# Optimization experiments

Hardware: AMD Instinct MI355X
Metric: run time of the kernel (lower is better)

Reference implementation:

```python
import jax, jax.numpy as jnp
import numpy as np

B, S, D, H, MLP = 2, 2048, 1024, 16, 4096
DH = D // H
EPS_LN = 1e-6
KERNEL_EPS = 1e-3  # fast_attention generalized kernel_epsilon


def layer_norm(x, scale, bias):
    m = jnp.mean(x, axis=-1, keepdims=True)
    v = jnp.mean(jnp.square(x - m), axis=-1, keepdims=True)
    return (x - m) * jax.lax.rsqrt(v + EPS_LN) * scale + bias


def performer_causal_attention(q, k, v):
    """FAVOR+ generalized attention (deterministic relu features), causal.

    q,k,v: [B,S,H,DH]. phi(x) = relu(x) + eps. Linear-time via prefix sums:
      out_i = phi(q_i) . cumsum_j<=i phi(k_j) v_j^T / (phi(q_i) . cumsum phi(k_j))
    """
    phi_q = jax.nn.relu(q) + KERNEL_EPS          # [B,S,H,M]
    phi_k = jax.nn.relu(k) + KERNEL_EPS          # [B,S,H,M]
    kv = jnp.cumsum(jnp.einsum('bshm,bshd->bshmd', phi_k, v), axis=1)  # [B,S,H,M,DH]
    num = jnp.einsum('bshm,bshmd->bshd', phi_q, kv)
    den = jnp.einsum('bshm,bshm->bsh', phi_q, jnp.cumsum(phi_k, axis=1))
    return num / den[..., None]


def setup_inputs() -> dict:
    key = jax.random.key(0)
    ks = jax.random.split(key, 7)
    def w(k, shape, scale):
        return jax.random.normal(k, shape, jnp.float32) * scale
    s_in = 1.0 / np.sqrt(D)
    return {
        'inputs': jax.random.normal(ks[0], (B, S, D), jnp.float32),
        'ln1_scale': jnp.ones((D,), jnp.float32),
        'ln1_bias': jnp.zeros((D,), jnp.float32),
        'wq': w(ks[1], (D, H, DH), s_in),
        'wk': w(ks[2], (D, H, DH), s_in),
        'wv': w(ks[3], (D, H, DH), s_in),
        'wo': w(ks[4], (H, DH, D), s_in),
        'ln2_scale': jnp.ones((D,), jnp.float32),
        'ln2_bias': jnp.zeros((D,), jnp.float32),
        'w1': w(ks[5], (D, MLP), s_in),
        'b1': jnp.zeros((MLP,), jnp.float32),
        'w2': w(ks[6], (MLP, D), 1.0 / np.sqrt(MLP)),
        'b2': jnp.zeros((D,), jnp.float32),
    }


def reference(inputs, ln1_scale, ln1_bias, wq, wk, wv, wo,
              ln2_scale, ln2_bias, w1, b1, w2, b2):
    # pre-LN self-attention (Performer FAVOR+ generalized, causal)
    x = layer_norm(inputs, ln1_scale, ln1_bias)
    q = jnp.einsum('bsd,dhm->bshm', x, wq)
    k = jnp.einsum('bsd,dhm->bshm', x, wk)
    v = jnp.einsum('bsd,dhm->bshm', x, wv)
    attn = performer_causal_attention(q, k, v)          # [B,S,H,DH]
    attn_out = jnp.einsum('bshm,hmd->bsd', attn, wo)    # output projection
    x = attn_out + inputs                               # residual
    # pre-LN MLP block
    y = layer_norm(x, ln2_scale, ln2_bias)
    y = jax.nn.gelu(y @ w1 + b1) @ w2 + b2
    return x + y
```

## Files before the change

kernel.cpp:

```cpp
#include <hip/hip_runtime.h>
#include <math.h>
#include <stdint.h>

typedef __bf16 bf16;
typedef bf16  bf16x8 __attribute__((ext_vector_type(8)));
typedef float f32x4  __attribute__((ext_vector_type(4)));

constexpr int Bb  = 2;
constexpr int Ss  = 2048;
constexpr int Dd  = 1024;
constexpr int Hh  = 16;
constexpr int DHh = 64;
constexpr int MLPd = 4096;
constexpr int ROWS = Bb * Ss;
constexpr int NC  = Ss / 64;
constexpr int BH  = Bb * Hh;
constexpr float EPS_LN = 1e-6f;
constexpr float KEPS   = 1e-3f;

__device__ __forceinline__ void async_copy16(const bf16* g, bf16* l) {
    __builtin_amdgcn_global_load_lds(
        (__attribute__((address_space(1))) void*)g,
        (__attribute__((address_space(3))) void*)l,
        16, 0, 0);
}

__device__ __forceinline__ int swz64(int row, int col) {
    return row * 64 + (((col >> 3) ^ row) & 7) * 8 + (col & 7);
}

__global__ __launch_bounds__(256) void preproc_kernel(
    const float* __restrict__ inputs,
    const float* __restrict__ ln1_scale, const float* __restrict__ ln1_bias,
    bf16* __restrict__ xln, bf16* __restrict__ inp_bf,
    const float* __restrict__ wq, const float* __restrict__ wk,
    const float* __restrict__ wv, const float* __restrict__ wo,
    bf16* __restrict__ wqT, bf16* __restrict__ wkT,
    bf16* __restrict__ wvT, bf16* __restrict__ woT,
    const float* __restrict__ w1, bf16* __restrict__ w1T,
    const float* __restrict__ w2, bf16* __restrict__ w2T)
{
    __shared__ float tile[32][33];
    __shared__ float ssum[4], ssq[4];
    const int blk = blockIdx.x;
    const int sector = blk >> 12;

    if (sector == 0) {
        const int row = blk;
        const float* xr = inputs + (size_t)row * Dd;
        const int c0 = threadIdx.x * 4;
        float vals[4];
        float sum = 0.f, sumsq = 0.f;
#pragma unroll
        for (int i = 0; i < 4; i++) {
            float v = xr[c0 + i];
            vals[i] = v;
            sum += v;
            sumsq += v * v;
        }
#pragma unroll
        for (int off = 32; off > 0; off >>= 1) {
            sum   += __shfl_down(sum, off);
            sumsq += __shfl_down(sumsq, off);
        }
        const int wave = threadIdx.x >> 6;
        if ((threadIdx.x & 63) == 0) { ssum[wave] = sum; ssq[wave] = sumsq; }
        __syncthreads();
        const float tot   = ssum[0] + ssum[1] + ssum[2] + ssum[3];
        const float totsq = ssq[0] + ssq[1] + ssq[2] + ssq[3];
        const float mean = tot * (1.f / Dd);
        const float var  = totsq * (1.f / Dd) - mean * mean;
        const float r = rsqrtf(var + EPS_LN);
        bf16* orow = xln + (size_t)row * Dd;
        bf16* irow = inp_bf + (size_t)row * Dd;
#pragma unroll
        for (int i = 0; i < 4; i++) {
            irow[c0 + i] = (bf16)vals[i];
            orow[c0 + i] = (bf16)((vals[i] - mean) * r * ln1_scale[c0 + i] + ln1_bias[c0 + i]);
        }
    } else {
        const float* in; bf16* out; int K, N, bx, by;
        if (sector == 1) {
            const int local = blk - 4096;
            const int z = local >> 10;
            in  = (z == 0) ? wq : (z == 1) ? wk : (z == 2) ? wv : wo;
            out = (z == 0) ? wqT : (z == 1) ? wkT : (z == 2) ? wvT : woT;
            K = 1024; N = 1024;
            bx = local & 31; by = (local >> 5) & 31;
        } else if (sector == 2) {
            const int local = blk - 8192;
            in = w1; out = w1T; K = 1024; N = 4096;
            bx = local & 127; by = local >> 7;
        } else {
            const int local = blk - 12288;
            in = w2; out = w2T; K = 4096; N = 1024;
            bx = local & 31; by = local >> 5;
        }
        const int k0 = by * 32, n0 = bx * 32;
        const int tx = threadIdx.x & 31, ty = threadIdx.x >> 5;
#pragma unroll
        for (int i = 0; i < 32; i += 8)
            tile[ty + i][tx] = in[(size_t)(k0 + ty + i) * N + n0 + tx];
        __syncthreads();
#pragma unroll
        for (int i = 0; i < 32; i += 8)
            out[(size_t)(n0 + ty + i) * K + k0 + tx] = (bf16)tile[tx][ty + i];
    }
}

__global__ __launch_bounds__(256) void wo_reduce_ln(
    const float* __restrict__ psA, const float* __restrict__ psB,
    const bf16* __restrict__ inp,
    const float* __restrict__ scale, const float* __restrict__ bias,
    bf16* __restrict__ x2, bf16* __restrict__ yln)
{
    const int row = blockIdx.x;
    const int c0 = threadIdx.x * 4;
    const size_t base = (size_t)row * Dd + c0;
    float vals[4];
    float sum = 0.f, sumsq = 0.f;
#pragma unroll
    for (int i = 0; i < 4; i++) {
        float v = psA[base + i] + psB[base + i] + (float)inp[base + i];
        v = (float)(bf16)v;
        vals[i] = v;
        sum += v;
        sumsq += v * v;
    }
#pragma unroll
    for (int off = 32; off > 0; off >>= 1) {
        sum   += __shfl_down(sum, off);
        sumsq += __shfl_down(sumsq, off);
    }
    __shared__ float ssum[4], ssq[4];
    const int wave = threadIdx.x >> 6;
    if ((threadIdx.x & 63) == 0) { ssum[wave] = sum; ssq[wave] = sumsq; }
    __syncthreads();
    const float tot   = ssum[0] + ssum[1] + ssum[2] + ssum[3];
    const float totsq = ssq[0] + ssq[1] + ssq[2] + ssq[3];
    const float mean = tot * (1.f / Dd);
    const float var  = totsq * (1.f / Dd) - mean * mean;
    const float r = rsqrtf(var + EPS_LN);
#pragma unroll
    for (int i = 0; i < 4; i++) {
        x2[base + i]  = (bf16)vals[i];
        yln[base + i] = (bf16)((vals[i] - mean) * r * scale[c0 + i] + bias[c0 + i]);
    }
}

__global__ __launch_bounds__(256) void mlp2_reduce(
    float* __restrict__ outp, const float* __restrict__ psB,
    const float* __restrict__ b2, const bf16* __restrict__ x2)
{
    const size_t i4 = ((size_t)blockIdx.x * 256 + threadIdx.x) * 4;
    const int col = (int)(i4 & 1023);
    f32x4 a = *(const f32x4*)&outp[i4];
    f32x4 b = *(const f32x4*)&psB[i4];
    f32x4 o;
#pragma unroll
    for (int j = 0; j < 4; j++)
        o[j] = a[j] + b[j] + b2[col + j] + (float)x2[i4 + j];
    *(f32x4*)&outp[i4] = o;
}

enum { EP_QKV = 0, EP_NONE = 1, EP_RES = 2, EP_GELU = 3, EP_BIAS_RES = 4, EP_PARTIAL = 5 };

template <int TN, int BK, int NDIM, int KDIM, int MODE, int KSPLIT>
__global__ __launch_bounds__(256, 2) void mfma_gemm(const bf16* __restrict__ A,
                                                    const bf16* __restrict__ BT,
                                                    void* __restrict__ Cout,
                                                    const float* __restrict__ bias,
                                                    const void* __restrict__ res,
                                                    bf16* __restrict__ out2,
                                                    bf16* __restrict__ out3)
{
    constexpr int WCT = TN / 2;
    constexpr int NJ  = TN / 32;
    constexpr int NS  = BK / 32;
    constexpr int CPR = BK / 8;
    constexpr int RPI = 2048 / BK;
    constexpr int GRIDY = 32;
    constexpr int RPX = GRIDY / 8;
    constexpr int TILES = GRIDY * (NDIM / TN);
    constexpr int KLEN  = KDIM / KSPLIT;
    __shared__ bf16 As[128 * BK];
    __shared__ bf16 Bs[TN * BK];
    const int t = threadIdx.x;
    const int wave = t >> 6, lane = t & 63;

    const int bid0 = blockIdx.x;
    const int ks  = (KSPLIT > 1) ? (bid0 / TILES) : 0;
    const int bid = (KSPLIT > 1) ? (bid0 % TILES) : bid0;
    const int xcd = bid & 7, idx = bid >> 3;
    const int row0 = (xcd * RPX + (idx & (RPX - 1))) * 128;
    const int col0 = (idx / RPX) * TN;

    const int wr = wave >> 1, wc = wave & 1;

    const int srow = t / CPR;
    const int gch  = (t % CPR) ^ (srow & 7);
    const int sdst = t * 8;

    const bf16* gA = A  + (size_t)(row0 + srow) * KDIM + ks * KLEN + gch * 8;
    const bf16* gB = BT + (size_t)(col0 + srow) * KDIM + ks * KLEN + gch * 8;

    const int m = lane & 15, quad = lane >> 4;
    const int mx7 = m & 7;

    f32x4 acc[4][NJ] = {};

    for (int k0 = 0; k0 < KLEN; k0 += BK) {
        __syncthreads();
#pragma unroll
        for (int i = 0; i < 128 / RPI; i++)
            async_copy16(gA + (size_t)i * RPI * KDIM, &As[i * 2048 + sdst]);
#pragma unroll
        for (int i = 0; i < TN / RPI; i++)
            async_copy16(gB + (size_t)i * RPI * KDIM, &Bs[i * 2048 + sdst]);
        __syncthreads();

#pragma unroll
        for (int s = 0; s < NS; s++) {
            const int pco = ((s * 4 + quad) ^ mx7) * 8;
            bf16x8 aF[4], bF[NJ];
#pragma unroll
            for (int i = 0; i < 4; i++)
                aF[i] = *(const bf16x8*)&As[(wr * 64 + i * 16 + m) * BK + pco];
#pragma unroll
            for (int j = 0; j < NJ; j++)
                bF[j] = *(const bf16x8*)&Bs[(wc * WCT + j * 16 + m) * BK + pco];
#pragma unroll
            for (int i = 0; i < 4; i++)
#pragma unroll
                for (int j = 0; j < NJ; j++)
                    acc[i][j] = __builtin_amdgcn_mfma_f32_16x16x32_bf16(
                        aF[i], bF[j], acc[i][j], 0, 0, 0);
        }
        gA += BK;
        gB += BK;
    }

#pragma unroll
    for (int i = 0; i < 4; i++) {
#pragma unroll
        for (int j = 0; j < NJ; j++) {
#pragma unroll
            for (int r = 0; r < 4; r++) {
                const int row = row0 + wr * 64 + i * 16 + quad * 4 + r;
                const int col = col0 + wc * WCT + j * 16 + m;
                float val = acc[i][j][r];
                if constexpr (MODE == EP_QKV) {
                    const int third = col >> 10;
                    bf16* dst = (third == 0) ? (bf16*)Cout : (third == 1) ? out2 : out3;
                    if (third < 2) val = fmaxf(val, 0.f) + KEPS;
                    dst[(size_t)row * 1024 + (col & 1023)] = (bf16)val;
                } else if constexpr (MODE == EP_NONE) {
                    ((bf16*)Cout)[(size_t)row * NDIM + col] = (bf16)val;
                } else if constexpr (MODE == EP_RES) {
                    val += (float)((const bf16*)res)[(size_t)row * NDIM + col];
                    ((bf16*)Cout)[(size_t)row * NDIM + col] = (bf16)val;
                } else if constexpr (MODE == EP_GELU) {
                    val += bias[col];
                    const float u = 0.7978845608028654f * (val + 0.044715f * val * val * val);
                    const float e = __expf(2.f * u);
                    val = val * (1.f - 1.f / (e + 1.f));
                    ((bf16*)Cout)[(size_t)row * NDIM + col] = (bf16)val;
                } else if constexpr (MODE == EP_BIAS_RES) {
                    val += bias[col] + (float)((const bf16*)res)[(size_t)row * NDIM + col];
                    ((float*)Cout)[(size_t)row * NDIM + col] = val;
                } else {
                    float* dst = (ks == 0) ? (float*)Cout : (float*)out2;
                    dst[(size_t)row * NDIM + col] = val;
                }
            }
        }
    }
}

__global__ __launch_bounds__(256) void chunk_kv_kernel(const bf16* __restrict__ phik,
                                                       const bf16* __restrict__ v,
                                                       bf16* __restrict__ kvs,
                                                       float* __restrict__ ksums)
{
    const int c = blockIdx.x, bh = blockIdx.y;
    const int b = bh >> 4, h = bh & 15;
    __shared__ bf16 Kt[64 * 64];
    __shared__ bf16 Vt[64 * 64];
    const int t = threadIdx.x;
    const int wave = t >> 6, lane = t & 63;
    const int m16 = lane & 15, quad = lane >> 4;
    const int wr = wave >> 1, wc = wave & 1;
    const int f = t & 63, s4 = t >> 6;

#pragma unroll
    for (int i = 0; i < 16; i++) {
        const int s = s4 + 4 * i;
        const size_t g = ((size_t)((b * Ss + c * 64 + s) * Hh + h)) * DHh + f;
        Kt[swz64(f, s)] = phik[g];
        Vt[swz64(f, s)] = v[g];
    }
    __syncthreads();

    f32x4 acc[2][2] = {};
#pragma unroll
    for (int ks = 0; ks < 2; ks++) {
        bf16x8 aF[2], bF[2];
#pragma unroll
        for (int i = 0; i < 2; i++)
            aF[i] = *(const bf16x8*)&Kt[swz64(wr * 32 + i * 16 + m16, ks * 32 + quad * 8)];
#pragma unroll
        for (int j = 0; j < 2; j++)
            bF[j] = *(const bf16x8*)&Vt[swz64(wc * 32 + j * 16 + m16, ks * 32 + quad * 8)];
#pragma unroll
        for (int i = 0; i < 2; i++)
#pragma unroll
            for (int j = 0; j < 2; j++)
                acc[i][j] = __builtin_amdgcn_mfma_f32_16x16x32_bf16(
                    aF[i], bF[j], acc[i][j], 0, 0, 0);
    }

    const size_t base = ((size_t)bh * NC + c) * 4096;
#pragma unroll
    for (int i = 0; i < 2; i++)
#pragma unroll
        for (int j = 0; j < 2; j++)
#pragma unroll
            for (int r = 0; r < 4; r++) {
                const int mrow = wr * 32 + i * 16 + quad * 4 + r;
                const int dcol = wc * 32 + j * 16 + m16;
                kvs[base + mrow * 64 + dcol] = (bf16)acc[i][j][r];
            }

    if (t < 64) {
        float s_ = 0.f;
#pragma unroll
        for (int p = 0; p < 8; p++) {
            bf16x8 k8 = *(const bf16x8*)&Kt[t * 64 + p * 8];
#pragma unroll
            for (int e = 0; e < 8; e++) s_ += (float)k8[e];
        }
        ksums[((size_t)bh * NC + c) * 64 + t] = s_;
    }
}

__global__ __launch_bounds__(256) void scan_kernel(bf16* __restrict__ kvs,
                                                   float* __restrict__ ksums)
{
    const int e  = blockIdx.x * 256 + threadIdx.x;
    const int bh = blockIdx.y;
    float run = 0.f;
#pragma unroll 4
    for (int c = 0; c < NC; c++) {
        const size_t idx = ((size_t)bh * NC + c) * 4096 + e;
        const float val = (float)kvs[idx];
        kvs[idx] = (bf16)run;
        run += val;
    }
    if (blockIdx.x == 0 && threadIdx.x < 64) {
        float r = 0.f;
        for (int c = 0; c < NC; c++) {
            const size_t idx = ((size_t)bh * NC + c) * 64 + threadIdx.x;
            const float val = ksums[idx];
            ksums[idx] = r;
            r += val;
        }
    }
}

__global__ __launch_bounds__(256) void attn_out_kernel(const bf16* __restrict__ phiq,
                                                       const bf16* __restrict__ phik,
                                                       const bf16* __restrict__ v,
                                                       const bf16* __restrict__ kvs,
                                                       const float* __restrict__ ksums,
                                                       bf16* __restrict__ attn)
{
    const int c = blockIdx.x, bh = blockIdx.y;
    const int b = bh >> 4, h = bh & 15;
    __shared__ bf16 Qs [64 * 64];
    __shared__ bf16 KVb[64 * 64];
    __shared__ bf16 Sm [64 * 64];
    __shared__ bf16 KVt[64 * 64];
    __shared__ float ksm[64], den[64];
    const int t = threadIdx.x;
    const int wave = t >> 6, lane = t & 63;
    const int m16 = lane & 15, quad = lane >> 4;
    const int wr = wave >> 1, wc = wave & 1;
    const int f = t & 63, s4 = t >> 6;

#pragma unroll
    for (int i = 0; i < 16; i++) {
        const int s = s4 + 4 * i;
        const size_t g = ((size_t)((b * Ss + c * 64 + s) * Hh + h)) * DHh + f;
        Qs [swz64(s, f)] = phiq[g];
        KVb[swz64(s, f)] = phik[g];
    }
    if (t < 64) ksm[t] = ksums[((size_t)bh * NC + c) * 64 + t];
    __syncthreads();

    f32x4 sacc[2][2] = {};
#pragma unroll
    for (int ks = 0; ks < 2; ks++) {
        bf16x8 aF[2], bF[2];
#pragma unroll
        for (int i = 0; i < 2; i++)
            aF[i] = *(const bf16x8*)&Qs [swz64(wr * 32 + i * 16 + m16, ks * 32 + quad * 8)];
#pragma unroll
        for (int j = 0; j < 2; j++)
            bF[j] = *(const bf16x8*)&KVb[swz64(wc * 32 + j * 16 + m16, ks * 32 + quad * 8)];
#pragma unroll
        for (int i = 0; i < 2; i++)
#pragma unroll
            for (int j = 0; j < 2; j++)
                sacc[i][j] = __builtin_amdgcn_mfma_f32_16x16x32_bf16(
                    aF[i], bF[j], sacc[i][j], 0, 0, 0);
    }
#pragma unroll
    for (int i = 0; i < 2; i++)
#pragma unroll
        for (int j = 0; j < 2; j++)
#pragma unroll
            for (int r = 0; r < 4; r++) {
                const int row = wr * 32 + i * 16 + quad * 4 + r;
                const int col = wc * 32 + j * 16 + m16;
                Sm[swz64(row, col)] = (bf16)((col <= row) ? sacc[i][j][r] : 0.f);
            }
    __syncthreads();

#pragma unroll
    for (int i = 0; i < 16; i++) {
        const int s = s4 + 4 * i;
        const size_t g = ((size_t)((b * Ss + c * 64 + s) * Hh + h)) * DHh + f;
        KVb[swz64(f, s)] = v[g];
    }
    {
        const size_t base = ((size_t)bh * NC + c) * 4096;
#pragma unroll
        for (int i = 0; i < 16; i++) {
            const int e = t + 256 * i;
            KVt[swz64(e & 63, e >> 6)] = kvs[base + e];
        }
    }
    __syncthreads();

    if (t < 64) {
        float d_ = 0.f;
#pragma unroll
        for (int p = 0; p < 8; p++) {
            const int gc = (p ^ (t & 7)) * 8;
            bf16x8 q8 = *(const bf16x8*)&Qs[t * 64 + p * 8];
            bf16x8 s8 = *(const bf16x8*)&Sm[t * 64 + p * 8];
#pragma unroll
            for (int e = 0; e < 8; e++)
                d_ += (float)q8[e] * ksm[gc + e] + (float)s8[e];
        }
        den[t] = d_;
    }

    f32x4 oacc[2][2] = {};
#pragma unroll
    for (int ks = 0; ks < 2; ks++) {
        bf16x8 aF[2], bF[2];
#pragma unroll
        for (int i = 0; i < 2; i++)
            aF[i] = *(const bf16x8*)&Sm [swz64(wr * 32 + i * 16 + m16, ks * 32 + quad * 8)];
#pragma unroll
        for (int j = 0; j < 2; j++)
            bF[j] = *(const bf16x8*)&KVb[swz64(wc * 32 + j * 16 + m16, ks * 32 + quad * 8)];
#pragma unroll
        for (int i = 0; i < 2; i++)
#pragma unroll
            for (int j = 0; j < 2; j++)
                oacc[i][j] = __builtin_amdgcn_mfma_f32_16x16x32_bf16(
                    aF[i], bF[j], oacc[i][j], 0, 0, 0);
    }
#pragma unroll
    for (int ks = 0; ks < 2; ks++) {
        bf16x8 aF[2], bF[2];
#pragma unroll
        for (int i = 0; i < 2; i++)
            aF[i] = *(const bf16x8*)&Qs [swz64(wr * 32 + i * 16 + m16, ks * 32 + quad * 8)];
#pragma unroll
        for (int j = 0; j < 2; j++)
            bF[j] = *(const bf16x8*)&KVt[swz64(wc * 32 + j * 16 + m16, ks * 32 + quad * 8)];
#pragma unroll
        for (int i = 0; i < 2; i++)
#pragma unroll
            for (int j = 0; j < 2; j++)
                oacc[i][j] = __builtin_amdgcn_mfma_f32_16x16x32_bf16(
                    aF[i], bF[j], oacc[i][j], 0, 0, 0);
    }
    __syncthreads();

#pragma unroll
    for (int i = 0; i < 2; i++) {
#pragma unroll
        for (int r = 0; r < 4; r++) {
            const int row = wr * 32 + i * 16 + quad * 4 + r;
            const float dinv = 1.f / den[row];
#pragma unroll
            for (int j = 0; j < 2; j++) {
                const int col = wc * 32 + j * 16 + m16;
                attn[((size_t)((b * Ss + c * 64 + row) * Hh + h)) * DHh + col] =
                    (bf16)(oacc[i][j][r] * dinv);
            }
        }
    }
}

extern "C" void kernel_launch(void* const* d_in, const int* in_sizes, int n_in,
                              void* d_out, int out_size, void* d_ws, size_t ws_size,
                              hipStream_t stream)
{
    const float* inputs    = (const float*)d_in[0];
    const float* ln1_scale = (const float*)d_in[1];
    const float* ln1_bias  = (const float*)d_in[2];
    const float* wq        = (const float*)d_in[3];
    const float* wk        = (const float*)d_in[4];
    const float* wv        = (const float*)d_in[5];
    const float* wo        = (const float*)d_in[6];
    const float* ln2_scale = (const float*)d_in[7];
    const float* ln2_bias  = (const float*)d_in[8];
    const float* w1        = (const float*)d_in[9];
    const float* b1        = (const float*)d_in[10];
    const float* w2        = (const float*)d_in[11];
    const float* b2        = (const float*)d_in[12];
    float* out = (float*)d_out;

    char* ws = (char*)d_ws;
    bf16*  xln    = (bf16*)ws;
    bf16*  q      = (bf16*)(ws + (8ull  << 20));
    bf16*  k      = (bf16*)(ws + (16ull << 20));
    bf16*  v      = (bf16*)(ws + (24ull << 20));
    bf16*  kvs    = (bf16*)(ws + (32ull << 20));
    bf16*  x2     = (bf16*)(ws + (48ull << 20));
    bf16*  inp_bf = (bf16*)(ws + (56ull << 20));
    float* ksums  = (float*)(ws + (64ull << 20));
    bf16*  wqT    = (bf16*)(ws + (64ull << 20) + (1ull << 18));
    bf16*  wkT    = wqT + 1024 * 1024;
    bf16*  wvT    = wkT + 1024 * 1024;
    bf16*  woT    = wvT + 1024 * 1024;
    bf16*  w1T    = woT + 1024 * 1024;
    bf16*  w2T    = w1T + 4096 * 1024;
    bf16*  attn   = xln;
    bf16*  yln    = q;
    bf16*  hbuf   = k;
    float* psWo0  = (float*)(ws + (16ull << 20));
    float* psWo1  = (float*)(ws + (32ull << 20));
    float* psM2   = (float*)ws;

    preproc_kernel<<<16384, 256, 0, stream>>>(
        inputs, ln1_scale, ln1_bias, xln, inp_bf,
        wq, wk, wv, wo, wqT, wkT, wvT, woT, w1, w1T, w2, w2T);

    mfma_gemm<128, 128, 3072, 1024, EP_QKV, 1><<<dim3(24 * 32), 256, 0, stream>>>(
        xln, wqT, q, nullptr, nullptr, k, v);

    {
        dim3 gridA(NC, BH);
        chunk_kv_kernel<<<gridA, 256, 0, stream>>>(k, v, kvs, ksums);
        scan_kernel<<<dim3(4096 / 256, BH), 256, 0, stream>>>(kvs, ksums);
        attn_out_kernel<<<gridA, 256, 0, stream>>>(q, k, v, kvs, ksums, attn);
    }

    mfma_gemm<128, 128, 1024, 1024, EP_PARTIAL, 2><<<dim3(512), 256, 0, stream>>>(
        attn, woT, psWo0, nullptr, nullptr, (bf16*)psWo1, nullptr);

    wo_reduce_ln<<<ROWS, 256, 0, stream>>>(psWo0, psWo1, inp_bf,
                                           ln2_scale, ln2_bias, x2, yln);

    mfma_gemm<128, 128, 4096, 1024, EP_GELU, 1><<<dim3(32 * 32), 256, 0, stream>>>(
        yln, w1T, hbuf, b1, nullptr, nullptr, nullptr);

    mfma_gemm<128, 128, 1024, 4096, EP_PARTIAL, 2><<<dim3(512), 256, 0, stream>>>(
        hbuf, w2T, out, nullptr, nullptr, (bf16*)psM2, nullptr);

    mlp2_reduce<<<4096, 256, 0, stream>>>(out, psM2, b2, x2);
}
```

Before: 299.0 us.

## Drop split-K for Wo GEMM with fused residual; retile MLP GEMMs

New measurement: 297.6 us. About the same (-0.5%).

```diff
diff --git a/kernel.cpp b/kernel.cpp
--- a/kernel.cpp
+++ b/kernel.cpp
@@ -108,21 +108,19 @@
     }
 }
 
-__global__ __launch_bounds__(256) void wo_reduce_ln(
-    const float* __restrict__ psA, const float* __restrict__ psB,
-    const bf16* __restrict__ inp,
-    const float* __restrict__ scale, const float* __restrict__ bias,
-    bf16* __restrict__ x2, bf16* __restrict__ yln)
+__global__ __launch_bounds__(256) void ln_kernel(const bf16* __restrict__ x,
+                                                 const float* __restrict__ scale,
+                                                 const float* __restrict__ bias,
+                                                 bf16* __restrict__ out)
 {
     const int row = blockIdx.x;
+    const bf16* xr = x + (size_t)row * Dd;
     const int c0 = threadIdx.x * 4;
-    const size_t base = (size_t)row * Dd + c0;
     float vals[4];
     float sum = 0.f, sumsq = 0.f;
 #pragma unroll
     for (int i = 0; i < 4; i++) {
-        float v = psA[base + i] + psB[base + i] + (float)inp[base + i];
-        v = (float)(bf16)v;
+        float v = (float)xr[c0 + i];
         vals[i] = v;
         sum += v;
         sumsq += v * v;
@@ -141,11 +139,10 @@
     const float mean = tot * (1.f / Dd);
     const float var  = totsq * (1.f / Dd) - mean * mean;
     const float r = rsqrtf(var + EPS_LN);
-#pragma unroll
-    for (int i = 0; i < 4; i++) {
-        x2[base + i]  = (bf16)vals[i];
-        yln[base + i] = (bf16)((vals[i] - mean) * r * scale[c0 + i] + bias[c0 + i]);
-    }
+    bf16* orow = out + (size_t)row * Dd;
+#pragma unroll
+    for (int i = 0; i < 4; i++)
+        orow[c0 + i] = (bf16)((vals[i] - mean) * r * scale[c0 + i] + bias[c0 + i]);
 }
 
 __global__ __launch_bounds__(256) void mlp2_reduce(
@@ -544,8 +541,6 @@
     bf16*  attn   = xln;
     bf16*  yln    = q;
     bf16*  hbuf   = k;
-    float* psWo0  = (float*)(ws + (16ull << 20));
-    float* psWo1  = (float*)(ws + (32ull << 20));
     float* psM2   = (float*)ws;
 
     preproc_kernel<<<16384, 256, 0, stream>>>(
@@ -562,16 +557,15 @@
         attn_out_kernel<<<gridA, 256, 0, stream>>>(q, k, v, kvs, ksums, attn);
     }
 
-    mfma_gemm<128, 128, 1024, 1024, EP_PARTIAL, 2><<<dim3(512), 256, 0, stream>>>(
-        attn, woT, psWo0, nullptr, nullptr, (bf16*)psWo1, nullptr);
-
-    wo_reduce_ln<<<ROWS, 256, 0, stream>>>(psWo0, psWo1, inp_bf,
-                                           ln2_scale, ln2_bias, x2, yln);
-
-    mfma_gemm<128, 128, 4096, 1024, EP_GELU, 1><<<dim3(32 * 32), 256, 0, stream>>>(
+    mfma_gemm<64, 128, 1024, 1024, EP_RES, 1><<<dim3(512), 256, 0, stream>>>(
+        attn, woT, x2, nullptr, inp_bf, nullptr, nullptr);
+
+    ln_kernel<<<ROWS, 256, 0, stream>>>(x2, ln2_scale, ln2_bias, yln);
+
+    mfma_gemm<256, 64, 4096, 1024, EP_GELU, 1><<<dim3(16 * 32), 256, 0, stream>>>(
         yln, w1T, hbuf, b1, nullptr, nullptr, nullptr);
 
-    mfma_gemm<128, 128, 1024, 4096, EP_PARTIAL, 2><<<dim3(512), 256, 0, stream>>>(
+    mfma_gemm<128, 64, 1024, 4096, EP_PARTIAL, 2><<<dim3(512), 256, 0, stream>>>(
         hbuf, w2T, out, nullptr, nullptr, (bf16*)psM2, nullptr);
 
     mlp2_reduce<<<4096, 256, 0, stream>>>(out, psM2, b2, x2);
```
